# Performance work log

Measured on AMD Instinct MI355X. Metric: run time of the kernel, lower is better.

## Reference

```python
import jax, jax.numpy as jnp
import numpy as np

B, S, H, I, E, TOP_K = 2, 2048, 768, 3072, 7, 2


def setup_inputs() -> dict:
    key = jax.random.key(0)
    ks = jax.random.split(key, 5)
    x = jax.random.normal(ks[0], (B, S, H), dtype=jnp.float32)
    # parameter init ~ torch Linear default scale (1/sqrt(fan_in))
    wg = jax.random.normal(ks[1], (H, E), dtype=jnp.float32) / np.sqrt(H)
    bg = jnp.zeros((E,), dtype=jnp.float32)
    w1 = jax.random.normal(ks[2], (E, H, I), dtype=jnp.float32) / np.sqrt(H)
    b1 = jnp.zeros((E, I), dtype=jnp.float32)
    w2 = jax.random.normal(ks[3], (E, I, H), dtype=jnp.float32) / np.sqrt(I)
    b2 = jnp.zeros((E, H), dtype=jnp.float32)
    return {"x": x, "wg": wg, "bg": bg, "w1": w1, "b1": b1, "w2": w2, "b2": b2}


def _gate_weights(gate_logits):
    # top-k mask: -inf everywhere except top-k slots, then softmax.
    # Equivalent: softmax over top-k values, scattered back into [.., E].
    vals, idx = jax.lax.top_k(gate_logits, TOP_K)           # [B,S,K]
    wk = jax.nn.softmax(vals, axis=-1)                       # [B,S,K]
    onehot = jax.nn.one_hot(idx, E, dtype=gate_logits.dtype)  # [B,S,K,E]
    return jnp.einsum('bsk,bske->bse', wk, onehot)           # [B,S,E]


def reference(x, wg, bg, w1, b1, w2, b2):
    gate_logits = jnp.einsum('bsh,he->bse', x, wg) + bg      # [B,S,E]
    gate_w = _gate_weights(gate_logits)                       # [B,S,E]
    # dense all-expert FFN (the module evaluates EVERY expert on every token)
    h = jnp.einsum('bsh,ehi->bsei', x, w1) + b1              # [B,S,E,I]
    h = jax.nn.gelu(h, approximate=False)                    # torch.nn.GELU (exact erf)
    expert_out = jnp.einsum('bsei,eih->bseh', h, w2) + b2    # [B,S,E,H]
    out = jnp.einsum('bseh,bse->bsh', expert_out, gate_w)    # weighted combine
    # dropout is identity in eval mode
    return (out, gate_w)
```

## Files before the change

### kernel.cpp

```cpp
#include <hip/hip_runtime.h>
#include <hip/hip_bf16.h>
#include <cmath>

#define NT 4096
#define HD 768
#define ID 3072
#define NE 7
#define NP 8192
#define TM 256
#define TN 256
#define BK 32
#define KS 2
#define NT2 (HD / TN)
#define SLOTS 102
#define NRING 4
#define FFN1_MT 39
#define FFN1_NT (ID / TN)
#define FFN1_GRID (FFN1_NT * FFN1_MT)

using short8 = __attribute__((ext_vector_type(8))) short;
using f32x4  = __attribute__((ext_vector_type(4))) float;
typedef __hip_bfloat16 bf16;

typedef const __attribute__((address_space(1))) void* gas_ptr;
typedef __attribute__((address_space(3))) void* las_ptr;
#define GLDS(g, l) __builtin_amdgcn_global_load_lds((gas_ptr)(g), (las_ptr)(l), 16, 0, 0)

#define BAR()   asm volatile("s_barrier" ::: "memory")
#define WAITL() asm volatile("s_waitcnt lgkmcnt(0)" ::: "memory")
#define WV8()   asm volatile("s_waitcnt vmcnt(8)" ::: "memory")
#define WV4()   asm volatile("s_waitcnt vmcnt(4)" ::: "memory")
#define WV0()   asm volatile("s_waitcnt vmcnt(0)" ::: "memory")
#define SCHEDB() __builtin_amdgcn_sched_barrier(0)

__device__ inline float b2f(unsigned short u) {
  unsigned v = (unsigned)u << 16; float f; __builtin_memcpy(&f, &v, 4); return f;
}

__device__ inline float gelu_erf(float v) {
  float xa = fabsf(v) * 0.70710678118654752f;
  float t  = __builtin_amdgcn_rcpf(1.0f + 0.3275911f * xa);
  float p  = t * (0.254829592f + t * (-0.284496736f + t * (1.421413741f +
             t * (-1.453152027f + t * 1.061405429f))));
  float er = 1.0f - p * __expf(-xa * xa);
  er = (v < 0.0f) ? -er : er;
  return 0.5f * v * (1.0f + er);
}

__global__ __launch_bounds__(64) void gate_kernel(
    const float* __restrict__ x, const float* __restrict__ wg, const float* __restrict__ bg,
    float* __restrict__ gate_out, bf16* __restrict__ xb,
    float* __restrict__ pair_w, int* __restrict__ tokexp)
{
  int t = blockIdx.x;
  int lane = threadIdx.x;
  const float* xr = x + (size_t)t * HD;
  float acc[NE];
#pragma unroll
  for (int e = 0; e < NE; e++) acc[e] = 0.f;
#pragma unroll
  for (int j = 0; j < HD / 64; j++) {
    int h = lane + j * 64;
    float xv = xr[h];
    xb[(size_t)t * HD + h] = __float2bfloat16(xv);
    const float* wr = wg + (size_t)h * NE;
#pragma unroll
    for (int e = 0; e < NE; e++) acc[e] += xv * wr[e];
  }
#pragma unroll
  for (int e = 0; e < NE; e++) {
    float v = acc[e];
    for (int s = 32; s > 0; s >>= 1) v += __shfl_down(v, s, 64);
    acc[e] = v;
  }
  if (lane == 0) {
    float lg[NE];
#pragma unroll
    for (int e = 0; e < NE; e++) lg[e] = acc[e] + bg[e];
    int i0 = 0;
    for (int e = 1; e < NE; e++) if (lg[e] > lg[i0]) i0 = e;
    int i1 = -1;
    for (int e = 0; e < NE; e++) {
      if (e == i0) continue;
      if (i1 < 0 || lg[e] > lg[i1]) i1 = e;
    }
    float v0 = lg[i0], v1 = lg[i1];
    float e1 = expf(v1 - v0);
    float inv = 1.f / (1.f + e1);
    float w0 = inv, w1v = e1 * inv;
    float* go = gate_out + (size_t)t * NE;
#pragma unroll
    for (int e = 0; e < NE; e++) go[e] = 0.f;
    go[i0] = w0; go[i1] = w1v;
    pair_w[2 * t + 0] = w0;
    pair_w[2 * t + 1] = w1v;
    tokexp[2 * t + 0] = i0;
    tokexp[2 * t + 1] = i1;
  }
}

__global__ __launch_bounds__(256) void route_kernel(
    const int* __restrict__ tokexp, int* __restrict__ elist, int* __restrict__ counts)
{
  __shared__ int wcnt[4];
  int e = blockIdx.x;
  int tid = threadIdx.x, wv = tid >> 6, ln = tid & 63;
  int base = 0;
  for (int chunk = 0; chunk < NP; chunk += 256) {
    int p = chunk + tid;
    bool m = (tokexp[p] == e);
    unsigned long long bal = __ballot(m);
    if (ln == 0) wcnt[wv] = __popcll(bal);
    __syncthreads();
    int pre = 0;
#pragma unroll
    for (int w = 0; w < 4; w++) pre += (w < wv) ? wcnt[w] : 0;
    int rank = pre + __popcll(bal & ((1ull << ln) - 1ull));
    if (m) elist[e * NP + base + rank] = p;
    base += wcnt[0] + wcnt[1] + wcnt[2] + wcnt[3];
    __syncthreads();
  }
  if (tid == 0) counts[e] = base;
}

__global__ __launch_bounds__(256) void transpose_cvt_kernel(
    const float* __restrict__ src, bf16* __restrict__ dst, int K, int N)
{
  __shared__ float tile[64][65];
  int e = blockIdx.z;
  int n0 = blockIdx.x * 64;
  int k0 = blockIdx.y * 64;
  const float* s = src + (size_t)e * K * N;
  bf16* d = dst + (size_t)e * K * N;
  int t = threadIdx.x;
  {
    int kk = t >> 4;
    int nc = (t & 15) << 2;
#pragma unroll
    for (int r = 0; r < 4; r++) {
      int k = kk + r * 16;
      float4 v = *(const float4*)(s + (size_t)(k0 + k) * N + n0 + nc);
      tile[k][nc + 0] = v.x; tile[k][nc + 1] = v.y;
      tile[k][nc + 2] = v.z; tile[k][nc + 3] = v.w;
    }
  }
  __syncthreads();
  {
    int c = t & 15;
    int nbase = t >> 4;
#pragma unroll
    for (int r = 0; r < 4; r++) {
      int n = nbase + r * 16;
      bf16 tmp[4];
#pragma unroll
      for (int i = 0; i < 4; i++) tmp[i] = __float2bfloat16(tile[4 * c + i][n]);
      ushort4 u; __builtin_memcpy(&u, tmp, 8);
      *(ushort4*)(d + (size_t)(n0 + n) * K + k0 + 4 * c) = u;
    }
  }
}


__global__ __launch_bounds__(512, 2) void ffn1_kernel(
    const bf16* __restrict__ xb, const bf16* __restrict__ w1t, const float* __restrict__ b1,
    const int* __restrict__ counts, const int* __restrict__ elist, bf16* __restrict__ hbuf)
{
  __shared__ bf16 As[NRING][TM][4][8];
  __shared__ bf16 Bs[NRING][TN][4][8];
  __shared__ int plist[TM];

  int tid = threadIdx.x;
  int raw = blockIdx.x;
  int xcd = raw & 7, pos = raw >> 3;
  int v = (xcd < 4) ? xcd * 59 + pos : 236 + (xcd - 4) * 58 + pos;
  int by = v / FFN1_NT, bx = v % FFN1_NT;

  int e, base = 0, cnt = 0, acct = 0;
  bool found = false;
  for (e = 0; e < NE; e++) {
    cnt = counts[e];
    int tiles = (cnt + TM - 1) / TM;
    if (by < acct + tiles) { base = (by - acct) * TM; found = true; break; }
    acct += tiles;
  }
  if (!found) return;

  if (tid < TM) {
    int r = base + tid;
    plist[tid] = (r < cnt) ? elist[e * NP + r] : -1;
  }
  __syncthreads();

  const int n0 = bx * TN;
  const bf16* Bsrc = w1t + (size_t)e * ID * HD;

  int c0 = tid, c1 = tid + 512;
  int r0 = c0 >> 2, k0 = (c0 & 3) ^ ((r0 >> 1) & 3);
  int r1 = c1 >> 2, k1 = (c1 & 3) ^ ((r1 >> 1) & 3);
  int pr0 = plist[r0], pr1 = plist[r1];
  const bf16* a0 = xb + (size_t)((pr0 >= 0 ? pr0 : 0) >> 1) * HD + k0 * 8;
  const bf16* a1 = xb + (size_t)((pr1 >= 0 ? pr1 : 0) >> 1) * HD + k1 * 8;
  const bf16* b0 = Bsrc + (size_t)(n0 + r0) * HD + k0 * 8;
  const bf16* b1v = Bsrc + (size_t)(n0 + r1) * HD + k1 * 8;

#define STAGE_A(t_) do { bf16* d_ = (bf16*)As + (size_t)((t_) & 3) * TM * 32;    \
    GLDS(a0 + (size_t)(t_) * BK, d_ + c0 * 8);                                   \
    GLDS(a1 + (size_t)(t_) * BK, d_ + c1 * 8); } while (0)
#define STAGE_B(t_) do { bf16* d_ = (bf16*)Bs + (size_t)((t_) & 3) * TN * 32;    \
    GLDS(b0 + (size_t)(t_) * BK, d_ + c0 * 8);                                   \
    GLDS(b1v + (size_t)(t_) * BK, d_ + c1 * 8); } while (0)

  int wave = tid >> 6, lane = tid & 63;
  int wm = (wave >> 2) * 128, wn = (wave & 3) * 64;
  int lr = lane & 15, quad = lane >> 4;
  int ph = quad ^ ((lr >> 1) & 3);

  f32x4 acc[8][4] = {};
  const int NIT = HD / BK;

  STAGE_A(0); STAGE_B(0);
  STAGE_A(1); STAGE_B(1);
  STAGE_A(2); STAGE_B(2);
  WV8(); BAR();

  for (int t = 0; t < NIT; ++t) {
    int q = t & 3;
    short8 af[4], bfr[4];
#pragma unroll
    for (int mi = 0; mi < 4; mi++) af[mi] = *(const short8*)&As[q][wm + mi * 16 + lr][ph][0];
#pragma unroll
    for (int nj = 0; nj < 4; nj++) bfr[nj] = *(const short8*)&Bs[q][wn + nj * 16 + lr][ph][0];
    if (t + 3 < NIT) STAGE_A(t + 3);
    BAR();
    WAITL(); SCHEDB();
    __builtin_amdgcn_s_setprio(1);
#pragma unroll
    for (int mi = 0; mi < 4; mi++)
#pragma unroll
      for (int nj = 0; nj < 4; nj++)
        acc[mi][nj] = __builtin_amdgcn_mfma_f32_16x16x32_bf16(bfr[nj], af[mi], acc[mi][nj], 0, 0, 0);
    __builtin_amdgcn_s_setprio(0);
    BAR();
#pragma unroll
    for (int mi = 0; mi < 4; mi++) af[mi] = *(const short8*)&As[q][wm + 64 + mi * 16 + lr][ph][0];
    if (t + 3 < NIT) STAGE_B(t + 3);
    if (t + 3 < NIT) { WV8(); } else if (t + 2 < NIT) { WV4(); } else if (t + 1 < NIT) { WV0(); }
    BAR();
    WAITL(); SCHEDB();
    __builtin_amdgcn_s_setprio(1);
#pragma unroll
    for (int mi = 0; mi < 4; mi++)
#pragma unroll
      for (int nj = 0; nj < 4; nj++)
        acc[4 + mi][nj] = __builtin_amdgcn_mfma_f32_16x16x32_bf16(bfr[nj], af[mi], acc[4 + mi][nj], 0, 0, 0);
    __builtin_amdgcn_s_setprio(0);
    BAR();
  }
#undef STAGE_A
#undef STAGE_B

  const float* b1e = b1 + (size_t)e * ID;
#pragma unroll
  for (int mi = 0; mi < 8; mi++) {
    int mrow = wm + mi * 16 + lr;
    int p = plist[mrow];
    if (p >= 0) {
      bf16* drow = hbuf + (size_t)p * ID;
#pragma unroll
      for (int nj = 0; nj < 4; nj++) {
        int colb = n0 + wn + nj * 16 + (quad << 2);
        float4 bs = *(const float4*)(b1e + colb);
        bf16 o[4];
        o[0] = __float2bfloat16(gelu_erf(acc[mi][nj][0] + bs.x));
        o[1] = __float2bfloat16(gelu_erf(acc[mi][nj][1] + bs.y));
        o[2] = __float2bfloat16(gelu_erf(acc[mi][nj][2] + bs.z));
        o[3] = __float2bfloat16(gelu_erf(acc[mi][nj][3] + bs.w));
        ushort4 u; __builtin_memcpy(&u, o, 8);
        *(ushort4*)(drow + colb) = u;
      }
    }
  }
}

__global__ __launch_bounds__(512, 2) void ffn2_kernel(
    const bf16* __restrict__ hbuf, const bf16* __restrict__ w2t, const float* __restrict__ b2,
    const int* __restrict__ counts, const int* __restrict__ elist,
    const float* __restrict__ pair_w, bf16* __restrict__ pout)
{
  __shared__ bf16 As[NRING][TM][4][8];
  __shared__ bf16 Bs[NRING][TN][4][8];
  __shared__ int plist[TM];

  int tid = threadIdx.x;
  int xcd = blockIdx.x;
  int slot = blockIdx.y;
  int e = 0, seg = 0, base = 0, cnt = 0, n0 = 0;
  bool found = false;
  for (int p = xcd; p < 2 * NE; p += 8) {
    int pe = p >> 1;
    int c = counts[pe];
    int tiles = ((c + TM - 1) / TM) * NT2;
    if (slot < tiles) {
      e = pe; seg = p & 1; cnt = c;
      base = (slot / NT2) * TM;
      n0 = (slot % NT2) * TN;
      found = true; break;
    }
    slot -= tiles;
  }
  if (!found) return;

  if (tid < TM) {
    int r = base + tid;
    plist[tid] = (r < cnt) ? elist[e * NP + r] : -1;
  }
  __syncthreads();

  const int kbase = seg * (ID / KS);
  const bf16* Bsrc = w2t + (size_t)e * HD * ID;

  int c0 = tid, c1 = tid + 512;
  int r0 = c0 >> 2, k0 = (c0 & 3) ^ ((r0 >> 1) & 3);
  int r1 = c1 >> 2, k1 = (c1 & 3) ^ ((r1 >> 1) & 3);
  int pr0 = plist[r0], pr1 = plist[r1];
  const bf16* a0 = hbuf + (size_t)(pr0 >= 0 ? pr0 : 0) * ID + kbase + k0 * 8;
  const bf16* a1 = hbuf + (size_t)(pr1 >= 0 ? pr1 : 0) * ID + kbase + k1 * 8;
  const bf16* b0 = Bsrc + (size_t)(n0 + r0) * ID + kbase + k0 * 8;
  const bf16* b1v = Bsrc + (size_t)(n0 + r1) * ID + kbase + k1 * 8;

#define STAGE_A(t_) do { bf16* d_ = (bf16*)As + (size_t)((t_) & 3) * TM * 32;    \
    GLDS(a0 + (size_t)(t_) * BK, d_ + c0 * 8);                                   \
    GLDS(a1 + (size_t)(t_) * BK, d_ + c1 * 8); } while (0)
#define STAGE_B(t_) do { bf16* d_ = (bf16*)Bs + (size_t)((t_) & 3) * TN * 32;    \
    GLDS(b0 + (size_t)(t_) * BK, d_ + c0 * 8);                                   \
    GLDS(b1v + (size_t)(t_) * BK, d_ + c1 * 8); } while (0)

  int wave = tid >> 6, lane = tid & 63;
  int wm = (wave >> 2) * 128, wn = (wave & 3) * 64;
  int lr = lane & 15, quad = lane >> 4;
  int ph = quad ^ ((lr >> 1) & 3);

  f32x4 acc[8][4] = {};
  const int NIT = (ID / KS) / BK;

  STAGE_A(0); STAGE_B(0);
  STAGE_A(1); STAGE_B(1);
  STAGE_A(2); STAGE_B(2);
  WV8(); BAR();

  for (int t = 0; t < NIT; ++t) {
    int q = t & 3;
    short8 af[4], bfr[4];
#pragma unroll
    for (int mi = 0; mi < 4; mi++) af[mi] = *(const short8*)&As[q][wm + mi * 16 + lr][ph][0];
#pragma unroll
    for (int nj = 0; nj < 4; nj++) bfr[nj] = *(const short8*)&Bs[q][wn + nj * 16 + lr][ph][0];
    if (t + 3 < NIT) STAGE_A(t + 3);
    BAR();
    WAITL(); SCHEDB();
    __builtin_amdgcn_s_setprio(1);
#pragma unroll
    for (int mi = 0; mi < 4; mi++)
#pragma unroll
      for (int nj = 0; nj < 4; nj++)
        acc[mi][nj] = __builtin_amdgcn_mfma_f32_16x16x32_bf16(bfr[nj], af[mi], acc[mi][nj], 0, 0, 0);
    __builtin_amdgcn_s_setprio(0);
    BAR();
#pragma unroll
    for (int mi = 0; mi < 4; mi++) af[mi] = *(const short8*)&As[q][wm + 64 + mi * 16 + lr][ph][0];
    if (t + 3 < NIT) STAGE_B(t + 3);
    if (t + 3 < NIT) { WV8(); } else if (t + 2 < NIT) { WV4(); } else if (t + 1 < NIT) { WV0(); }
    BAR();
    WAITL(); SCHEDB();
    __builtin_amdgcn_s_setprio(1);
#pragma unroll
    for (int mi = 0; mi < 4; mi++)
#pragma unroll
      for (int nj = 0; nj < 4; nj++)
        acc[4 + mi][nj] = __builtin_amdgcn_mfma_f32_16x16x32_bf16(bfr[nj], af[mi], acc[4 + mi][nj], 0, 0, 0);
    __builtin_amdgcn_s_setprio(0);
    BAR();
  }
#undef STAGE_A
#undef STAGE_B

  const float* b2e = b2 + (size_t)e * HD;
#pragma unroll
  for (int mi = 0; mi < 8; mi++) {
    int mrow = wm + mi * 16 + lr;
    int p = plist[mrow];
    if (p >= 0) {
      float pw = pair_w[p];
      bf16* drow = pout + ((size_t)seg * NP + p) * HD;
#pragma unroll
      for (int nj = 0; nj < 4; nj++) {
        int colb = n0 + wn + nj * 16 + (quad << 2);
        float bx_ = 0.f, by_ = 0.f, bz_ = 0.f, bw_ = 0.f;
        if (seg == 0) {
          float4 bs = *(const float4*)(b2e + colb);
          bx_ = bs.x; by_ = bs.y; bz_ = bs.z; bw_ = bs.w;
        }
        bf16 o[4];
        o[0] = __float2bfloat16((acc[mi][nj][0] + bx_) * pw);
        o[1] = __float2bfloat16((acc[mi][nj][1] + by_) * pw);
        o[2] = __float2bfloat16((acc[mi][nj][2] + bz_) * pw);
        o[3] = __float2bfloat16((acc[mi][nj][3] + bw_) * pw);
        ushort4 u; __builtin_memcpy(&u, o, 8);
        *(ushort4*)(drow + colb) = u;
      }
    }
  }
}

__global__ __launch_bounds__(192) void combine_kernel(
    const bf16* __restrict__ pout, float* __restrict__ out)
{
  int t = blockIdx.x, j = threadIdx.x;
  f32x4 o = {0.f, 0.f, 0.f, 0.f};
#pragma unroll
  for (int s = 0; s < KS; s++) {
#pragma unroll
    for (int k = 0; k < 2; k++) {
      const ushort4* v = (const ushort4*)(pout + ((size_t)s * NP + 2 * t + k) * HD);
      ushort4 u = v[j];
      o[0] += b2f(u.x); o[1] += b2f(u.y); o[2] += b2f(u.z); o[3] += b2f(u.w);
    }
  }
  ((f32x4*)(out + (size_t)t * HD))[j] = o;
}

extern "C" void kernel_launch(void* const* d_in, const int* in_sizes, int n_in,
                              void* d_out, int out_size, void* d_ws, size_t ws_size,
                              hipStream_t stream)
{
  const float* x  = (const float*)d_in[0];
  const float* wg = (const float*)d_in[1];
  const float* bg = (const float*)d_in[2];
  const float* w1 = (const float*)d_in[3];
  const float* b1 = (const float*)d_in[4];
  const float* w2 = (const float*)d_in[5];
  const float* b2 = (const float*)d_in[6];
  float* out = (float*)d_out;
  float* gate_out = out + (size_t)NT * HD;

  char* ws = (char*)d_ws;
  size_t off = 0;
  int* counts  = (int*)(ws + off);  off += 256;
  int* tokexp  = (int*)(ws + off);  off += (size_t)NP * 4;
  int* elist   = (int*)(ws + off);  off += (size_t)NE * NP * 4;
  float* pair_w = (float*)(ws + off); off += (size_t)NP * 4;
  bf16* xb   = (bf16*)(ws + off);   off += (size_t)NT * HD * 2;
  bf16* w1t  = (bf16*)(ws + off);   off += (size_t)NE * HD * ID * 2;
  bf16* w2t  = (bf16*)(ws + off);   off += (size_t)NE * HD * ID * 2;
  bf16* hbuf = (bf16*)(ws + off);   off += (size_t)NP * ID * 2;
  bf16* pout = (bf16*)(ws + off);   off += (size_t)KS * NP * HD * 2;

  gate_kernel<<<NT, 64, 0, stream>>>(x, wg, bg, gate_out, xb, pair_w, tokexp);
  route_kernel<<<NE, 256, 0, stream>>>(tokexp, elist, counts);
  transpose_cvt_kernel<<<dim3(ID / 64, HD / 64, NE), 256, 0, stream>>>(w1, w1t, HD, ID);
  transpose_cvt_kernel<<<dim3(HD / 64, ID / 64, NE), 256, 0, stream>>>(w2, w2t, ID, HD);
  ffn1_kernel<<<FFN1_GRID, 512, 0, stream>>>(xb, w1t, b1, counts, elist, hbuf);
  ffn2_kernel<<<dim3(8, SLOTS), 512, 0, stream>>>(hbuf, w2t, b2, counts, elist, pair_w, pout);
  combine_kernel<<<NT, 192, 0, stream>>>(pout, out);
}
```

Before: 330.8 us.

## Fuse prep kernels and replace combine pass with atomic accumulation in ffn2

Merges gating, bf16 conversion and both weight transposes into one launch that also zeroes the output buffer. The second FFN now atomically adds its weighted results into the fp32 output, removing the intermediate bf16 partial buffer and the separate combine kernel. This cuts launches and intermediate memory traffic, at the cost of scalar float atomics and non-deterministic summation order.

Result: slower. 465.0 us (+40.6%).

```diff
diff --git a/kernel.cpp b/kernel.cpp
--- a/kernel.cpp
+++ b/kernel.cpp
@@ -18,6 +18,10 @@
 #define FFN1_NT (ID / TN)
 #define FFN1_GRID (FFN1_NT * FFN1_MT)
 
+#define G_GATE 1024
+#define G_TR1  (48 * 12 * NE)
+#define G_TR2  (12 * 48 * NE)
+
 using short8 = __attribute__((ext_vector_type(8))) short;
 using f32x4  = __attribute__((ext_vector_type(4))) float;
 typedef __hip_bfloat16 bf16;
@@ -47,55 +51,111 @@
   return 0.5f * v * (1.0f + er);
 }
 
-__global__ __launch_bounds__(64) void gate_kernel(
+__device__ inline void transpose_body(const float* __restrict__ s, bf16* __restrict__ d,
+                                      int K, int N, int n0, int k0, int t,
+                                      float (*tile)[65]) {
+  {
+    int kk = t >> 4;
+    int nc = (t & 15) << 2;
+#pragma unroll
+    for (int r = 0; r < 4; r++) {
+      int k = kk + r * 16;
+      float4 v = *(const float4*)(s + (size_t)(k0 + k) * N + n0 + nc);
+      tile[k][nc + 0] = v.x; tile[k][nc + 1] = v.y;
+      tile[k][nc + 2] = v.z; tile[k][nc + 3] = v.w;
+    }
+  }
+  __syncthreads();
+  {
+    int c = t & 15;
+    int nbase = t >> 4;
+#pragma unroll
+    for (int r = 0; r < 4; r++) {
+      int n = nbase + r * 16;
+      bf16 tmp[4];
+#pragma unroll
+      for (int i = 0; i < 4; i++) tmp[i] = __float2bfloat16(tile[4 * c + i][n]);
+      ushort4 u; __builtin_memcpy(&u, tmp, 8);
+      *(ushort4*)(d + (size_t)(n0 + n) * K + k0 + 4 * c) = u;
+    }
+  }
+}
+
+__global__ __launch_bounds__(256) void prep_kernel(
     const float* __restrict__ x, const float* __restrict__ wg, const float* __restrict__ bg,
-    float* __restrict__ gate_out, bf16* __restrict__ xb,
-    float* __restrict__ pair_w, int* __restrict__ tokexp)
+    const float* __restrict__ w1, const float* __restrict__ w2,
+    float* __restrict__ gate_out, float* __restrict__ out, bf16* __restrict__ xb,
+    float* __restrict__ pair_w, int* __restrict__ tokexp,
+    bf16* __restrict__ w1t, bf16* __restrict__ w2t)
 {
-  int t = blockIdx.x;
-  int lane = threadIdx.x;
-  const float* xr = x + (size_t)t * HD;
-  float acc[NE];
-#pragma unroll
-  for (int e = 0; e < NE; e++) acc[e] = 0.f;
-#pragma unroll
-  for (int j = 0; j < HD / 64; j++) {
-    int h = lane + j * 64;
-    float xv = xr[h];
-    xb[(size_t)t * HD + h] = __float2bfloat16(xv);
-    const float* wr = wg + (size_t)h * NE;
-#pragma unroll
-    for (int e = 0; e < NE; e++) acc[e] += xv * wr[e];
-  }
-#pragma unroll
-  for (int e = 0; e < NE; e++) {
-    float v = acc[e];
-    for (int s = 32; s > 0; s >>= 1) v += __shfl_down(v, s, 64);
-    acc[e] = v;
-  }
-  if (lane == 0) {
-    float lg[NE];
-#pragma unroll
-    for (int e = 0; e < NE; e++) lg[e] = acc[e] + bg[e];
-    int i0 = 0;
-    for (int e = 1; e < NE; e++) if (lg[e] > lg[i0]) i0 = e;
-    int i1 = -1;
+  __shared__ float tile[64][65];
+  int b = blockIdx.x;
+  int tid = threadIdx.x;
+
+  if (b < G_GATE) {
+    int wavei = tid >> 6, lane = tid & 63;
+    int t = b * 4 + wavei;
+    const float* xr = x + (size_t)t * HD;
+    float acc[NE];
+#pragma unroll
+    for (int e = 0; e < NE; e++) acc[e] = 0.f;
+#pragma unroll
+    for (int j = 0; j < HD / 64; j++) {
+      int h = lane + j * 64;
+      float xv = xr[h];
+      xb[(size_t)t * HD + h] = __float2bfloat16(xv);
+      const float* wr = wg + (size_t)h * NE;
+#pragma unroll
+      for (int e = 0; e < NE; e++) acc[e] += xv * wr[e];
+    }
+    f32x4 z = {0.f, 0.f, 0.f, 0.f};
+#pragma unroll
+    for (int jj = 0; jj < 3; jj++)
+      ((f32x4*)(out + (size_t)t * HD))[lane + jj * 64] = z;
+#pragma unroll
     for (int e = 0; e < NE; e++) {
-      if (e == i0) continue;
-      if (i1 < 0 || lg[e] > lg[i1]) i1 = e;
-    }
-    float v0 = lg[i0], v1 = lg[i1];
-    float e1 = expf(v1 - v0);
-    float inv = 1.f / (1.f + e1);
-    float w0 = inv, w1v = e1 * inv;
-    float* go = gate_out + (size_t)t * NE;
-#pragma unroll
-    for (int e = 0; e < NE; e++) go[e] = 0.f;
-    go[i0] = w0; go[i1] = w1v;
-    pair_w[2 * t + 0] = w0;
-    pair_w[2 * t + 1] = w1v;
-    tokexp[2 * t + 0] = i0;
-    tokexp[2 * t + 1] = i1;
+      float v = acc[e];
+      for (int s = 32; s > 0; s >>= 1) v += __shfl_down(v, s, 64);
+      acc[e] = v;
+    }
+    if (lane == 0) {
+      float lg[NE];
+#pragma unroll
+      for (int e = 0; e < NE; e++) lg[e] = acc[e] + bg[e];
+      int i0 = 0;
+      for (int e = 1; e < NE; e++) if (lg[e] > lg[i0]) i0 = e;
+      int i1 = -1;
+      for (int e = 0; e < NE; e++) {
+        if (e == i0) continue;
+        if (i1 < 0 || lg[e] > lg[i1]) i1 = e;
+      }
+      float v0 = lg[i0], v1 = lg[i1];
+      float e1 = expf(v1 - v0);
+      float inv = 1.f / (1.f + e1);
+      float w0 = inv, w1v = e1 * inv;
+      float* go = gate_out + (size_t)t * NE;
+#pragma unroll
+      for (int e = 0; e < NE; e++) go[e] = 0.f;
+      go[i0] = w0; go[i1] = w1v;
+      pair_w[2 * t + 0] = w0;
+      pair_w[2 * t + 1] = w1v;
+      tokexp[2 * t + 0] = i0;
+      tokexp[2 * t + 1] = i1;
+    }
+  } else if (b < G_GATE + G_TR1) {
+    int id = b - G_GATE;
+    int e = id / (48 * 12);
+    int rem = id % (48 * 12);
+    int bx = rem % 48, by = rem / 48;
+    transpose_body(w1 + (size_t)e * HD * ID, w1t + (size_t)e * HD * ID,
+                   HD, ID, bx * 64, by * 64, tid, tile);
+  } else {
+    int id = b - G_GATE - G_TR1;
+    int e = id / (12 * 48);
+    int rem = id % (12 * 48);
+    int bx = rem % 12, by = rem / 12;
+    transpose_body(w2 + (size_t)e * ID * HD, w2t + (size_t)e * ID * HD,
+                   ID, HD, bx * 64, by * 64, tid, tile);
   }
 }
 
@@ -123,43 +183,6 @@
   if (tid == 0) counts[e] = base;
 }
 
-__global__ __launch_bounds__(256) void transpose_cvt_kernel(
-    const float* __restrict__ src, bf16* __restrict__ dst, int K, int N)
-{
-  __shared__ float tile[64][65];
-  int e = blockIdx.z;
-  int n0 = blockIdx.x * 64;
-  int k0 = blockIdx.y * 64;
-  const float* s = src + (size_t)e * K * N;
-  bf16* d = dst + (size_t)e * K * N;
-  int t = threadIdx.x;
-  {
-    int kk = t >> 4;
-    int nc = (t & 15) << 2;
-#pragma unroll
-    for (int r = 0; r < 4; r++) {
-      int k = kk + r * 16;
-      float4 v = *(const float4*)(s + (size_t)(k0 + k) * N + n0 + nc);
-      tile[k][nc + 0] = v.x; tile[k][nc + 1] = v.y;
-      tile[k][nc + 2] = v.z; tile[k][nc + 3] = v.w;
-    }
-  }
-  __syncthreads();
-  {
-    int c = t & 15;
-    int nbase = t >> 4;
-#pragma unroll
-    for (int r = 0; r < 4; r++) {
-      int n = nbase + r * 16;
-      bf16 tmp[4];
-#pragma unroll
-      for (int i = 0; i < 4; i++) tmp[i] = __float2bfloat16(tile[4 * c + i][n]);
-      ushort4 u; __builtin_memcpy(&u, tmp, 8);
-      *(ushort4*)(d + (size_t)(n0 + n) * K + k0 + 4 * c) = u;
-    }
-  }
-}
-
 
 __global__ __launch_bounds__(512, 2) void ffn1_kernel(
     const bf16* __restrict__ xb, const bf16* __restrict__ w1t, const float* __restrict__ b1,
@@ -285,7 +308,7 @@
 __global__ __launch_bounds__(512, 2) void ffn2_kernel(
     const bf16* __restrict__ hbuf, const bf16* __restrict__ w2t, const float* __restrict__ b2,
     const int* __restrict__ counts, const int* __restrict__ elist,
-    const float* __restrict__ pair_w, bf16* __restrict__ pout)
+    const float* __restrict__ pair_w, float* __restrict__ out)
 {
   __shared__ bf16 As[NRING][TM][4][8];
   __shared__ bf16 Bs[NRING][TN][4][8];
@@ -391,7 +414,7 @@
     int p = plist[mrow];
     if (p >= 0) {
       float pw = pair_w[p];
-      bf16* drow = pout + ((size_t)seg * NP + p) * HD;
+      float* orow = out + (size_t)(p >> 1) * HD;
 #pragma unroll
       for (int nj = 0; nj < 4; nj++) {
         int colb = n0 + wn + nj * 16 + (quad << 2);
@@ -400,33 +423,13 @@
           float4 bs = *(const float4*)(b2e + colb);
           bx_ = bs.x; by_ = bs.y; bz_ = bs.z; bw_ = bs.w;
         }
-        bf16 o[4];
-        o[0] = __float2bfloat16((acc[mi][nj][0] + bx_) * pw);
-        o[1] = __float2bfloat16((acc[mi][nj][1] + by_) * pw);
-        o[2] = __float2bfloat16((acc[mi][nj][2] + bz_) * pw);
-        o[3] = __float2bfloat16((acc[mi][nj][3] + bw_) * pw);
-        ushort4 u; __builtin_memcpy(&u, o, 8);
-        *(ushort4*)(drow + colb) = u;
+        atomicAdd(&orow[colb + 0], (acc[mi][nj][0] + bx_) * pw);
+        atomicAdd(&orow[colb + 1], (acc[mi][nj][1] + by_) * pw);
+        atomicAdd(&orow[colb + 2], (acc[mi][nj][2] + bz_) * pw);
+        atomicAdd(&orow[colb + 3], (acc[mi][nj][3] + bw_) * pw);
       }
     }
   }
-}
-
-__global__ __launch_bounds__(192) void combine_kernel(
-    const bf16* __restrict__ pout, float* __restrict__ out)
-{
-  int t = blockIdx.x, j = threadIdx.x;
-  f32x4 o = {0.f, 0.f, 0.f, 0.f};
-#pragma unroll
-  for (int s = 0; s < KS; s++) {
-#pragma unroll
-    for (int k = 0; k < 2; k++) {
-      const ushort4* v = (const ushort4*)(pout + ((size_t)s * NP + 2 * t + k) * HD);
-      ushort4 u = v[j];
-      o[0] += b2f(u.x); o[1] += b2f(u.y); o[2] += b2f(u.z); o[3] += b2f(u.w);
-    }
-  }
-  ((f32x4*)(out + (size_t)t * HD))[j] = o;
 }
 
 extern "C" void kernel_launch(void* const* d_in, const int* in_sizes, int n_in,
@@ -453,13 +456,10 @@
   bf16* w1t  = (bf16*)(ws + off);   off += (size_t)NE * HD * ID * 2;
   bf16* w2t  = (bf16*)(ws + off);   off += (size_t)NE * HD * ID * 2;
   bf16* hbuf = (bf16*)(ws + off);   off += (size_t)NP * ID * 2;
-  bf16* pout = (bf16*)(ws + off);   off += (size_t)KS * NP * HD * 2;
-
-  gate_kernel<<<NT, 64, 0, stream>>>(x, wg, bg, gate_out, xb, pair_w, tokexp);
+
+  prep_kernel<<<G_GATE + G_TR1 + G_TR2, 256, 0, stream>>>(
+      x, wg, bg, w1, w2, gate_out, out, xb, pair_w, tokexp, w1t, w2t);
   route_kernel<<<NE, 256, 0, stream>>>(tokexp, elist, counts);
-  transpose_cvt_kernel<<<dim3(ID / 64, HD / 64, NE), 256, 0, stream>>>(w1, w1t, HD, ID);
-  transpose_cvt_kernel<<<dim3(HD / 64, ID / 64, NE), 256, 0, stream>>>(w2, w2t, ID, HD);
   ffn1_kernel<<<FFN1_GRID, 512, 0, stream>>>(xb, w1t, b1, counts, elist, hbuf);
-  ffn2_kernel<<<dim3(8, SLOTS), 512, 0, stream>>>(hbuf, w2t, b2, counts, elist, pair_w, pout);
-  combine_kernel<<<NT, 192, 0, stream>>>(pout, out);
-}
+  ffn2_kernel<<<dim3(8, SLOTS), 512, 0, stream>>>(hbuf, w2t, b2, counts, elist, pair_w, out);
+}
```
